# Kernel tuning notes

Measured on AMD Instinct MI355X. Metric: run time of the kernel, lower is better.

Reference implementation:

```python
import jax, jax.numpy as jnp
import numpy as np

N = 70000
H = 8
E = 1120000
B = 8


def setup_inputs() -> dict:
    key = jax.random.key(0)
    ks = jax.random.split(key, 12)
    inp = {
        'calcium_t': jax.random.normal(ks[0], (B, N), jnp.float32),
        'hidden': jax.random.normal(ks[1], (B, N, H), jnp.float32),
        'src': jax.random.randint(ks[2], (E,), 0, N, jnp.int32),
        'tgt': jax.random.randint(ks[3], (E,), 0, N, jnp.int32),
        'W_z_values': jax.random.normal(ks[4], (E, H), jnp.float32) * 0.01,
        'W_r_values': jax.random.normal(ks[5], (E, H), jnp.float32) * 0.01,
        'W_h_values': jax.random.normal(ks[6], (E, H), jnp.float32) * 0.01,
        'U_z': jax.random.normal(ks[7], (N, H, H), jnp.float32) * 0.01,
        'U_r': jax.random.normal(ks[8], (N, H, H), jnp.float32) * 0.01,
        'U_h': jax.random.normal(ks[9], (N, H, H), jnp.float32) * 0.01,
        'b_z': jnp.zeros((N, H), jnp.float32),
        'b_r': jnp.zeros((N, H), jnp.float32),
        'b_h': jnp.zeros((N, H), jnp.float32),
        'output_projection': jax.random.normal(ks[10], (H,), jnp.float32),
    }
    return inp


def _sparse_matmul(values, src, tgt, calcium):
    # out[b, n, h] = sum over edges e with tgt[e]==n of values[e,h]*calcium[b,src[e]]
    # (identical to coalesced COO mm: duplicate (row,col) values are summed)
    gathered = calcium.T[src]                      # (E, B)
    contrib = gathered[:, :, None] * values[:, None, :]  # (E, B, H)
    out = jax.ops.segment_sum(contrib, tgt, num_segments=N)  # (N, B, H)
    return jnp.transpose(out, (1, 0, 2))           # (B, N, H)


def reference(calcium_t, hidden, src, tgt, W_z_values, W_r_values, W_h_values,
              U_z, U_r, U_h, b_z, b_r, b_h, output_projection):
    inp_z = _sparse_matmul(W_z_values, src, tgt, calcium_t)
    inp_r = _sparse_matmul(W_r_values, src, tgt, calcium_t)
    inp_h = _sparse_matmul(W_h_values, src, tgt, calcium_t)

    rec_z = jnp.einsum('bnh,nhi->bni', hidden, U_z)
    rec_r = jnp.einsum('bnh,nhi->bni', hidden, U_r)
    z = jax.nn.sigmoid(inp_z + rec_z + b_z[None])
    r = jax.nn.sigmoid(inp_r + rec_r + b_r[None])

    rec_h = jnp.einsum('bnh,nhi->bni', r * hidden, U_h)
    h_tilde = jnp.tanh(inp_h + rec_h + b_h[None])

    hidden_new = (1.0 - z) * hidden + z * h_tilde
    calcium_t1 = jax.nn.relu(jnp.einsum('bnh,h->bn', hidden_new, output_projection))
    return calcium_t1, hidden_new
```

## Files before the change

kernel.cpp:

```cpp
#include <hip/hip_runtime.h>


__device__ __forceinline__ float fast_sigmoid(float x) {
    return 1.0f / (1.0f + __expf(-x));
}
__device__ __forceinline__ float fast_tanh(float x) {
    return 2.0f / (1.0f + __expf(-2.0f * x)) - 1.0f;
}

__device__ __forceinline__ unsigned bfr(float x) {
    unsigned u = __float_as_uint(x);
    return (u + 0x7fffu + ((u >> 16) & 1u)) >> 16;
}
__device__ __forceinline__ uint4 pack8(float4 a, float4 b) {
    uint4 r;
    r.x = bfr(a.x) | (bfr(a.y) << 16);
    r.y = bfr(a.z) | (bfr(a.w) << 16);
    r.z = bfr(b.x) | (bfr(b.y) << 16);
    r.w = bfr(b.z) | (bfr(b.w) << 16);
    return r;
}

#define BFMA(acc, p, c)                                                        \
    {                                                                          \
        acc[0] += __uint_as_float((p).x << 16) * (c);                          \
        acc[1] += __uint_as_float((p).x & 0xffff0000u) * (c);                  \
        acc[2] += __uint_as_float((p).y << 16) * (c);                          \
        acc[3] += __uint_as_float((p).y & 0xffff0000u) * (c);                  \
        acc[4] += __uint_as_float((p).z << 16) * (c);                          \
        acc[5] += __uint_as_float((p).z & 0xffff0000u) * (c);                  \
        acc[6] += __uint_as_float((p).w << 16) * (c);                          \
        acc[7] += __uint_as_float((p).w & 0xffff0000u) * (c);                  \
    }

__global__ void hist_kernel(const int* __restrict__ tgt, int* __restrict__ cnt,
                            int* __restrict__ rank, const float* __restrict__ cal,
                            float* __restrict__ calT, int N, int E) {
    int i = blockIdx.x * blockDim.x + threadIdx.x;
    if (i <= N) {
        float4* o = (float4*)(calT + (size_t)i * 8);
        if (i == N) {
            o[0] = make_float4(0.f, 0.f, 0.f, 0.f);
            o[1] = make_float4(0.f, 0.f, 0.f, 0.f);
        } else {
            float v[8];
#pragma unroll
            for (int b = 0; b < 8; ++b) v[b] = cal[(size_t)b * N + i];
            o[0] = make_float4(v[0], v[1], v[2], v[3]);
            o[1] = make_float4(v[4], v[5], v[6], v[7]);
        }
    }
    int base = i * 4;
    if (base + 3 < E) {
        int4 t = *(const int4*)(tgt + base);
        int4 r;
        r.x = atomicAdd(&cnt[t.x], 1);
        r.y = atomicAdd(&cnt[t.y], 1);
        r.z = atomicAdd(&cnt[t.z], 1);
        r.w = atomicAdd(&cnt[t.w], 1);
        *(int4*)(rank + base) = r;
    } else {
        for (int k = base; k < E; ++k) rank[k] = atomicAdd(&cnt[tgt[k]], 1);
    }
}

__global__ __launch_bounds__(256) void alloc_kernel(const int* __restrict__ cnt,
                                                    int* __restrict__ rowBeg,
                                                    int* __restrict__ cursor, int N) {
    __shared__ int waveSum[4];
    const int n = blockIdx.x * 256 + threadIdx.x;
    const int lane = threadIdx.x & 63;
    const int wid = threadIdx.x >> 6;
    int c = (n < N) ? cnt[n] : 0;
    int pre = c;
#pragma unroll
    for (int off = 1; off < 64; off <<= 1) {
        int v = __shfl_up(pre, off, 64);
        if (lane >= off) pre += v;
    }
    if (lane == 63) waveSum[wid] = pre;
    __syncthreads();
    if (threadIdx.x == 0) {
        int s0 = waveSum[0], s1 = waveSum[1], s2 = waveSum[2], s3 = waveSum[3];
        int base = atomicAdd(cursor, s0 + s1 + s2 + s3);
        waveSum[0] = base;
        waveSum[1] = base + s0;
        waveSum[2] = base + s0 + s1;
        waveSum[3] = base + s0 + s1 + s2;
    }
    __syncthreads();
    if (n < N) rowBeg[n] = waveSum[wid] + (pre - c);
}

__global__ __launch_bounds__(256) void scatter_conv(
    const int* __restrict__ src, const int* __restrict__ tgt,
    const int* __restrict__ rank, const int* __restrict__ rowBeg,
    const float* __restrict__ Wz, const float* __restrict__ Wr,
    const float* __restrict__ Wh, uint4* __restrict__ recs,
    int* __restrict__ srcCSR, int E) {
    int gid = blockIdx.x * 256 + threadIdx.x;
    if (gid >= E) return;
    int pos = rowBeg[tgt[gid]] + rank[gid];
    const float4* wz4 = (const float4*)(Wz + (size_t)gid * 8);
    const float4* wr4 = (const float4*)(Wr + (size_t)gid * 8);
    const float4* wh4 = (const float4*)(Wh + (size_t)gid * 8);
    uint4 pz = pack8(wz4[0], wz4[1]);
    uint4 pr = pack8(wr4[0], wr4[1]);
    uint4 ph = pack8(wh4[0], wh4[1]);
    uint4* rp = recs + (size_t)pos * 3;
    rp[0] = pz;
    rp[1] = pr;
    rp[2] = ph;
    srcCSR[pos] = src[gid];
}

__device__ __forceinline__ float rscatter(float v[8], int lane) {
    const bool s0 = (lane & 8) != 0;
    const bool s1 = (lane & 16) != 0;
    const bool s2 = (lane & 32) != 0;
    float w0, w1, w2, w3, x0, x1;
    { float k = s0 ? v[1] : v[0], g = s0 ? v[0] : v[1]; w0 = k + __shfl_xor(g, 8, 64); }
    { float k = s0 ? v[3] : v[2], g = s0 ? v[2] : v[3]; w1 = k + __shfl_xor(g, 8, 64); }
    { float k = s0 ? v[5] : v[4], g = s0 ? v[4] : v[5]; w2 = k + __shfl_xor(g, 8, 64); }
    { float k = s0 ? v[7] : v[6], g = s0 ? v[6] : v[7]; w3 = k + __shfl_xor(g, 8, 64); }
    { float k = s1 ? w1 : w0, g = s1 ? w0 : w1; x0 = k + __shfl_xor(g, 16, 64); }
    { float k = s1 ? w3 : w2, g = s1 ? w2 : w3; x1 = k + __shfl_xor(g, 16, 64); }
    float k = s2 ? x1 : x0, g = s2 ? x0 : x1;
    return k + __shfl_xor(g, 32, 64);
}

__global__ __launch_bounds__(256) void gru_main(
    const float* __restrict__ calT, const float* __restrict__ hidden,
    const uint4* __restrict__ recs, const int* __restrict__ srcCSR,
    const float* __restrict__ Uz, const float* __restrict__ Ur,
    const float* __restrict__ Uh, const float* __restrict__ bz,
    const float* __restrict__ br, const float* __restrict__ bh,
    const float* __restrict__ proj, const int* __restrict__ rowBeg,
    const int* __restrict__ cnt,
    float* __restrict__ outCal, float* __restrict__ outHid, int N) {
    const int lane = threadIdx.x & 63;
    const int n = blockIdx.x * 4 + (threadIdx.x >> 6);
    if (n >= N) return;
    const int s = lane >> 3;
    const int b = lane & 7;

    const int start = rowBeg[n];
    const int end = start + cnt[n];

    const float hvS = hidden[((b * N + n) << 3) + s];

    float az[8] = {0, 0, 0, 0, 0, 0, 0, 0};
    float ar[8] = {0, 0, 0, 0, 0, 0, 0, 0};
    float ah[8] = {0, 0, 0, 0, 0, 0, 0, 0};

    for (int j = start + s; j < end; j += 8) {
        const uint4* rp = recs + (size_t)j * 3;
        uint4 pz = rp[0];
        uint4 pr = rp[1];
        uint4 ph = rp[2];
        float c = calT[(srcCSR[j] << 3) + b];
        BFMA(az, pz, c);
        BFMA(ar, pr, c);
        BFMA(ah, ph, c);
    }

    const int ub = (n << 6) + (s << 3);
    {
        float4 u0 = *(const float4*)(Uz + ub);
        float4 u1 = *(const float4*)(Uz + ub + 4);
        az[0] += hvS * u0.x; az[1] += hvS * u0.y; az[2] += hvS * u0.z; az[3] += hvS * u0.w;
        az[4] += hvS * u1.x; az[5] += hvS * u1.y; az[6] += hvS * u1.z; az[7] += hvS * u1.w;
    }
    {
        float4 u0 = *(const float4*)(Ur + ub);
        float4 u1 = *(const float4*)(Ur + ub + 4);
        ar[0] += hvS * u0.x; ar[1] += hvS * u0.y; ar[2] += hvS * u0.z; ar[3] += hvS * u0.w;
        ar[4] += hvS * u1.x; ar[5] += hvS * u1.y; ar[6] += hvS * u1.z; ar[7] += hvS * u1.w;
    }

    float AZ = rscatter(az, lane);
    float AR = rscatter(ar, lane);
    float z = fast_sigmoid(AZ + bz[(n << 3) + s]);
    float r = fast_sigmoid(AR + br[(n << 3) + s]);
    float rhS = r * hvS;

    {
        float4 u0 = *(const float4*)(Uh + ub);
        float4 u1 = *(const float4*)(Uh + ub + 4);
        ah[0] += rhS * u0.x; ah[1] += rhS * u0.y; ah[2] += rhS * u0.z; ah[3] += rhS * u0.w;
        ah[4] += rhS * u1.x; ah[5] += rhS * u1.y; ah[6] += rhS * u1.z; ah[7] += rhS * u1.w;
    }
    float AH = rscatter(ah, lane);
    float ht = fast_tanh(AH + bh[(n << 3) + s]);
    float hn = (1.0f - z) * hvS + z * ht;

    float cv = hn * proj[s];
    cv += __shfl_xor(cv, 8, 64);
    cv += __shfl_xor(cv, 16, 64);
    cv += __shfl_xor(cv, 32, 64);

    outHid[((b * N + n) << 3) + s] = hn;
    if (s == 0) outCal[b * N + n] = fmaxf(cv, 0.0f);
}

extern "C" void kernel_launch(void* const* d_in, const int* in_sizes, int n_in,
                              void* d_out, int out_size, void* d_ws, size_t ws_size,
                              hipStream_t stream) {
    const float* calcium = (const float*)d_in[0];
    const float* hidden  = (const float*)d_in[1];
    const int*   src     = (const int*)d_in[2];
    const int*   tgt     = (const int*)d_in[3];
    const float* Wz      = (const float*)d_in[4];
    const float* Wr      = (const float*)d_in[5];
    const float* Wh      = (const float*)d_in[6];
    const float* Uz      = (const float*)d_in[7];
    const float* Ur      = (const float*)d_in[8];
    const float* Uh      = (const float*)d_in[9];
    const float* bz      = (const float*)d_in[10];
    const float* br      = (const float*)d_in[11];
    const float* bh      = (const float*)d_in[12];
    const float* proj    = (const float*)d_in[13];

    const int E = in_sizes[2];
    const int H = in_sizes[13];
    const int N = in_sizes[10] / H;
    (void)n_in; (void)out_size; (void)ws_size;

    float* out = (float*)d_out;
    float* outCal = out;
    float* outHid = out + (size_t)in_sizes[0];

    char* ws = (char*)d_ws;
    int*   cnt    = (int*)ws;
    int*   cursor = (int*)(ws + (448 << 10));
    int*   rowBeg = (int*)(ws + (512 << 10));
    int*   rank   = (int*)(ws + (1 << 20));
    float* calT   = (float*)(ws + (6 << 20));
    int*   srcCSR = (int*)(ws + (9 << 20));
    uint4* recs   = (uint4*)(ws + (14 << 20));

    hipMemsetAsync(ws, 0, (448 << 10) + 4, stream);

    int histThreads = (E + 3) / 4;
    hist_kernel<<<(histThreads + 255) / 256, 256, 0, stream>>>(
        tgt, cnt, rank, calcium, calT, N, E);
    alloc_kernel<<<(N + 255) / 256, 256, 0, stream>>>(cnt, rowBeg, cursor, N);
    scatter_conv<<<(E + 255) / 256, 256, 0, stream>>>(
        src, tgt, rank, rowBeg, Wz, Wr, Wh, recs, srcCSR, E);
    gru_main<<<(N + 3) / 4, 256, 0, stream>>>(
        calT, hidden, recs, srcCSR, Uz, Ur, Uh, bz, br, bh, proj,
        rowBeg, cnt, outCal, outHid, N);
}
```

Measured before the change: 220.2 us.

## Pack source index into 64-byte edge records and hoist per-node loads

Each CSR edge record now holds the source index in a fourth 16-byte slot, so the record is 64 bytes and the separate srcCSR array disappears. The gather loop gets weights and index with one contiguous access instead of a dependent separate load. The scatter kernel handles two edges per thread with vectorized index loads. The U matrices and biases in gru_main are loaded before the edge loop so their latency overlaps it. The trade-off is a third more record bytes written and read, plus higher register pressure.

```diff
diff --git a/kernel.cpp b/kernel.cpp
--- a/kernel.cpp
+++ b/kernel.cpp
@@ -96,22 +96,40 @@
     const int* __restrict__ src, const int* __restrict__ tgt,
     const int* __restrict__ rank, const int* __restrict__ rowBeg,
     const float* __restrict__ Wz, const float* __restrict__ Wr,
-    const float* __restrict__ Wh, uint4* __restrict__ recs,
-    int* __restrict__ srcCSR, int E) {
-    int gid = blockIdx.x * 256 + threadIdx.x;
-    if (gid >= E) return;
-    int pos = rowBeg[tgt[gid]] + rank[gid];
-    const float4* wz4 = (const float4*)(Wz + (size_t)gid * 8);
-    const float4* wr4 = (const float4*)(Wr + (size_t)gid * 8);
-    const float4* wh4 = (const float4*)(Wh + (size_t)gid * 8);
-    uint4 pz = pack8(wz4[0], wz4[1]);
-    uint4 pr = pack8(wr4[0], wr4[1]);
-    uint4 ph = pack8(wh4[0], wh4[1]);
-    uint4* rp = recs + (size_t)pos * 3;
-    rp[0] = pz;
-    rp[1] = pr;
-    rp[2] = ph;
-    srcCSR[pos] = src[gid];
+    const float* __restrict__ Wh, uint4* __restrict__ recs, int E) {
+    int i0 = (blockIdx.x * 256 + threadIdx.x) * 2;
+    if (i0 + 1 < E) {
+        int2 t2 = *(const int2*)(tgt + i0);
+        int2 r2 = *(const int2*)(rank + i0);
+        int2 s2 = *(const int2*)(src + i0);
+        int posA = rowBeg[t2.x] + r2.x;
+        int posB = rowBeg[t2.y] + r2.y;
+        const float4* wzA = (const float4*)(Wz + (size_t)i0 * 8);
+        const float4* wrA = (const float4*)(Wr + (size_t)i0 * 8);
+        const float4* whA = (const float4*)(Wh + (size_t)i0 * 8);
+        uint4* rpA = recs + (size_t)posA * 4;
+        uint4* rpB = recs + (size_t)posB * 4;
+        rpA[0] = pack8(wzA[0], wzA[1]);
+        rpA[1] = pack8(wrA[0], wrA[1]);
+        rpA[2] = pack8(whA[0], whA[1]);
+        rpA[3] = make_uint4((unsigned)s2.x, 0, 0, 0);
+        rpB[0] = pack8(wzA[2], wzA[3]);
+        rpB[1] = pack8(wrA[2], wrA[3]);
+        rpB[2] = pack8(whA[2], whA[3]);
+        rpB[3] = make_uint4((unsigned)s2.y, 0, 0, 0);
+    } else {
+        for (int i = i0; i < E; ++i) {
+            int pos = rowBeg[tgt[i]] + rank[i];
+            const float4* wz4 = (const float4*)(Wz + (size_t)i * 8);
+            const float4* wr4 = (const float4*)(Wr + (size_t)i * 8);
+            const float4* wh4 = (const float4*)(Wh + (size_t)i * 8);
+            uint4* rp = recs + (size_t)pos * 4;
+            rp[0] = pack8(wz4[0], wz4[1]);
+            rp[1] = pack8(wr4[0], wr4[1]);
+            rp[2] = pack8(wh4[0], wh4[1]);
+            rp[3] = make_uint4((unsigned)src[i], 0, 0, 0);
+        }
+    }
 }
 
 __device__ __forceinline__ float rscatter(float v[8], int lane) {
@@ -131,7 +149,7 @@
 
 __global__ __launch_bounds__(256) void gru_main(
     const float* __restrict__ calT, const float* __restrict__ hidden,
-    const uint4* __restrict__ recs, const int* __restrict__ srcCSR,
+    const uint4* __restrict__ recs,
     const float* __restrict__ Uz, const float* __restrict__ Ur,
     const float* __restrict__ Uh, const float* __restrict__ bz,
     const float* __restrict__ br, const float* __restrict__ bh,
@@ -148,53 +166,52 @@
     const int end = start + cnt[n];
 
     const float hvS = hidden[((b * N + n) << 3) + s];
+    const int ub = (n << 6) + (s << 3);
+    float4 uz0 = *(const float4*)(Uz + ub);
+    float4 uz1 = *(const float4*)(Uz + ub + 4);
+    float4 ur0 = *(const float4*)(Ur + ub);
+    float4 ur1 = *(const float4*)(Ur + ub + 4);
+    float4 uh0 = *(const float4*)(Uh + ub);
+    float4 uh1 = *(const float4*)(Uh + ub + 4);
+    const float bzS = bz[(n << 3) + s];
+    const float brS = br[(n << 3) + s];
+    const float bhS = bh[(n << 3) + s];
+    const float pjS = proj[s];
 
     float az[8] = {0, 0, 0, 0, 0, 0, 0, 0};
     float ar[8] = {0, 0, 0, 0, 0, 0, 0, 0};
     float ah[8] = {0, 0, 0, 0, 0, 0, 0, 0};
 
     for (int j = start + s; j < end; j += 8) {
-        const uint4* rp = recs + (size_t)j * 3;
+        const uint4* rp = recs + (size_t)j * 4;
         uint4 pz = rp[0];
         uint4 pr = rp[1];
         uint4 ph = rp[2];
-        float c = calT[(srcCSR[j] << 3) + b];
+        uint4 sx = rp[3];
+        float c = calT[((int)sx.x << 3) + b];
         BFMA(az, pz, c);
         BFMA(ar, pr, c);
         BFMA(ah, ph, c);
     }
 
-    const int ub = (n << 6) + (s << 3);
-    {
-        float4 u0 = *(const float4*)(Uz + ub);
-        float4 u1 = *(const float4*)(Uz + ub + 4);
-        az[0] += hvS * u0.x; az[1] += hvS * u0.y; az[2] += hvS * u0.z; az[3] += hvS * u0.w;
-        az[4] += hvS * u1.x; az[5] += hvS * u1.y; az[6] += hvS * u1.z; az[7] += hvS * u1.w;
-    }
-    {
-        float4 u0 = *(const float4*)(Ur + ub);
-        float4 u1 = *(const float4*)(Ur + ub + 4);
-        ar[0] += hvS * u0.x; ar[1] += hvS * u0.y; ar[2] += hvS * u0.z; ar[3] += hvS * u0.w;
-        ar[4] += hvS * u1.x; ar[5] += hvS * u1.y; ar[6] += hvS * u1.z; ar[7] += hvS * u1.w;
-    }
+    az[0] += hvS * uz0.x; az[1] += hvS * uz0.y; az[2] += hvS * uz0.z; az[3] += hvS * uz0.w;
+    az[4] += hvS * uz1.x; az[5] += hvS * uz1.y; az[6] += hvS * uz1.z; az[7] += hvS * uz1.w;
+    ar[0] += hvS * ur0.x; ar[1] += hvS * ur0.y; ar[2] += hvS * ur0.z; ar[3] += hvS * ur0.w;
+    ar[4] += hvS * ur1.x; ar[5] += hvS * ur1.y; ar[6] += hvS * ur1.z; ar[7] += hvS * ur1.w;
 
     float AZ = rscatter(az, lane);
     float AR = rscatter(ar, lane);
-    float z = fast_sigmoid(AZ + bz[(n << 3) + s]);
-    float r = fast_sigmoid(AR + br[(n << 3) + s]);
+    float z = fast_sigmoid(AZ + bzS);
+    float r = fast_sigmoid(AR + brS);
     float rhS = r * hvS;
 
-    {
-        float4 u0 = *(const float4*)(Uh + ub);
-        float4 u1 = *(const float4*)(Uh + ub + 4);
-        ah[0] += rhS * u0.x; ah[1] += rhS * u0.y; ah[2] += rhS * u0.z; ah[3] += rhS * u0.w;
-        ah[4] += rhS * u1.x; ah[5] += rhS * u1.y; ah[6] += rhS * u1.z; ah[7] += rhS * u1.w;
-    }
+    ah[0] += rhS * uh0.x; ah[1] += rhS * uh0.y; ah[2] += rhS * uh0.z; ah[3] += rhS * uh0.w;
+    ah[4] += rhS * uh1.x; ah[5] += rhS * uh1.y; ah[6] += rhS * uh1.z; ah[7] += rhS * uh1.w;
     float AH = rscatter(ah, lane);
-    float ht = fast_tanh(AH + bh[(n << 3) + s]);
+    float ht = fast_tanh(AH + bhS);
     float hn = (1.0f - z) * hvS + z * ht;
 
-    float cv = hn * proj[s];
+    float cv = hn * pjS;
     cv += __shfl_xor(cv, 8, 64);
     cv += __shfl_xor(cv, 16, 64);
     cv += __shfl_xor(cv, 32, 64);
@@ -236,8 +253,7 @@
     int*   rowBeg = (int*)(ws + (512 << 10));
     int*   rank   = (int*)(ws + (1 << 20));
     float* calT   = (float*)(ws + (6 << 20));
-    int*   srcCSR = (int*)(ws + (9 << 20));
-    uint4* recs   = (uint4*)(ws + (14 << 20));
+    uint4* recs   = (uint4*)(ws + (9 << 20));
 
     hipMemsetAsync(ws, 0, (448 << 10) + 4, stream);
 
@@ -245,9 +261,9 @@
     hist_kernel<<<(histThreads + 255) / 256, 256, 0, stream>>>(
         tgt, cnt, rank, calcium, calT, N, E);
     alloc_kernel<<<(N + 255) / 256, 256, 0, stream>>>(cnt, rowBeg, cursor, N);
-    scatter_conv<<<(E + 255) / 256, 256, 0, stream>>>(
-        src, tgt, rank, rowBeg, Wz, Wr, Wh, recs, srcCSR, E);
+    scatter_conv<<<((E + 1) / 2 + 255) / 256, 256, 0, stream>>>(
+        src, tgt, rank, rowBeg, Wz, Wr, Wh, recs, E);
     gru_main<<<(N + 3) / 4, 256, 0, stream>>>(
-        calT, hidden, recs, srcCSR, Uz, Ur, Uh, bz, br, bh, proj,
+        calT, hidden, recs, Uz, Ur, Uh, bz, br, bh, proj,
         rowBeg, cnt, outCal, outHid, N);
 }
```

Result: faster. 201.4 us (-8.6%).
